# Kernel tuning notes

Measured on AMD Instinct MI355X. Metric: run time of the kernel, lower is better.

## Reference

```python
import jax, jax.numpy as jnp
import numpy as np

EPS = 1e-07
NUM_CLASSES = 46


def setup_inputs() -> dict:
    key = jax.random.key(0)
    k1, k2 = jax.random.split(key)
    N = 2_000_000
    y_pred = jax.random.uniform(k1, (N, NUM_CLASSES), dtype=jnp.float32)
    y_true = jax.random.randint(k2, (N,), 0, NUM_CLASSES, dtype=jnp.int64)
    return {"y_pred": y_pred, "y_true": y_true}


def reference(y_pred, y_true):
    # One fused pass replacing the 46-iteration Python loop.
    # onehot[n, c] = 1 if y_true[n] == c
    classes = jnp.arange(NUM_CLASSES, dtype=y_true.dtype)
    onehot = (y_true[:, None] == classes[None, :]).astype(y_pred.dtype)  # [N, C]

    col_sum = jnp.sum(y_pred, axis=0)                 # [C] = tp + fp per class
    tp = jnp.sum(onehot * y_pred, axis=0)             # [C]
    counts = jnp.sum(onehot, axis=0)                  # [C] = tp + fn per class

    fp = col_sum - tp
    fn = counts - tp

    precision = tp / (tp + fp + EPS)
    recall = tp / (tp + fn + EPS)
    f1 = 2.0 * precision * recall / (precision + recall + EPS)
    f1 = jnp.clip(f1, EPS, 1.0 - EPS)
    return 1.0 - jnp.mean(f1)
```

## Files before the change

kernel.cpp:

```cpp
#include <hip/hip_runtime.h>

#define EPSF 1e-7f
#define NCLS 46
#define BLOCK 256
#define GRID (23 * 72)

__global__ __launch_bounds__(BLOCK) void f1_partial(
    const float* __restrict__ yp,
    const int* __restrict__ yt,
    float* __restrict__ g_cs,
    float* __restrict__ g_tp,
    float* __restrict__ g_cnt,
    int n_rows)
{
    __shared__ float s_cs[NCLS], s_tp[NCLS], s_cnt[NCLS];
    const int tid = threadIdx.x;
    for (int i = tid; i < NCLS; i += BLOCK) { s_cs[i] = 0.f; s_tp[i] = 0.f; s_cnt[i] = 0.f; }
    __syncthreads();

    const int T  = BLOCK * GRID;
    const int t  = blockIdx.x * BLOCK + tid;
    const int s        = t % 23;
    const int rp0      = t / 23;
    const int rpstride = T / 23;
    const int npairs   = n_rows >> 1;

    int cls[4], hi[4];
    #pragma unroll
    for (int j = 0; j < 4; ++j) {
        int e  = 4 * s + j;
        hi[j]  = (e >= 46) ? 1 : 0;
        cls[j] = e - 46 * hi[j];
    }

    float cs[4] = {0.f,0.f,0.f,0.f};
    float tp[4] = {0.f,0.f,0.f,0.f};

    for (int rp = rp0; rp < npairs; rp += rpstride) {
        float4 v = *(const float4*)(yp + rp * 92 + 4 * s);
        int2 lab = *(const int2*)(yt + 2 * rp);
        float vv[4] = {v.x, v.y, v.z, v.w};
        #pragma unroll
        for (int j = 0; j < 4; ++j) {
            cs[j] += vv[j];
            int labj = hi[j] ? lab.y : lab.x;
            tp[j] += (labj == cls[j]) ? vv[j] : 0.f;
        }
    }

    #pragma unroll
    for (int j = 0; j < 4; ++j) {
        atomicAdd(&s_cs[cls[j]], cs[j]);
        atomicAdd(&s_tp[cls[j]], tp[j]);
    }

    for (int i = t; i < n_rows; i += T)
        atomicAdd(&s_cnt[yt[i]], 1.0f);

    if ((n_rows & 1) && blockIdx.x == 0 && tid < NCLS) {
        int L = n_rows - 1;
        float v = yp[L * NCLS + tid];
        atomicAdd(&s_cs[tid], v);
        if (yt[L] == tid) atomicAdd(&s_tp[tid], v);
    }

    __syncthreads();
    for (int i = tid; i < NCLS; i += BLOCK) {
        atomicAdd(&g_cs[i],  s_cs[i]);
        atomicAdd(&g_tp[i],  s_tp[i]);
        atomicAdd(&g_cnt[i], s_cnt[i]);
    }
}

__global__ void f1_final(const float* __restrict__ g_cs,
                         const float* __restrict__ g_tp,
                         const float* __restrict__ g_cnt,
                         float* __restrict__ out)
{
    const int lane = threadIdx.x;
    float f1 = 0.f;
    if (lane < NCLS) {
        float tp = g_tp[lane];
        float p  = tp / (g_cs[lane]  + EPSF);
        float r  = tp / (g_cnt[lane] + EPSF);
        float f  = 2.0f * p * r / (p + r + EPSF);
        f1 = fminf(fmaxf(f, EPSF), 1.0f - EPSF);
    }
    #pragma unroll
    for (int off = 32; off > 0; off >>= 1)
        f1 += __shfl_down(f1, off);
    if (lane == 0)
        out[0] = 1.0f - f1 * (1.0f / 46.0f);
}

extern "C" void kernel_launch(void* const* d_in, const int* in_sizes, int n_in,
                              void* d_out, int out_size, void* d_ws, size_t ws_size,
                              hipStream_t stream)
{
    const float* yp = (const float*)d_in[0];
    const int* yt   = (const int*)d_in[1];
    const int n_rows = in_sizes[1];

    float* g_cs  = (float*)d_ws;
    float* g_tp  = g_cs + NCLS;
    float* g_cnt = g_tp + NCLS;

    hipMemsetAsync(d_ws, 0, 3 * NCLS * sizeof(float), stream);
    f1_partial<<<GRID, BLOCK, 0, stream>>>(yp, yt, g_cs, g_tp, g_cnt, n_rows);
    f1_final<<<1, 64, 0, stream>>>(g_cs, g_tp, g_cnt, (float*)d_out);
}
```

Measured before the change: 524.0 us.

## Fuse finalize into reduction kernel via last-block ticket and inline label counting

Merges the final F1 computation into the partial-reduction kernel using a global atomic ticket, so the last block to finish computes the loss and the second kernel launch disappears. Label counts are now accumulated inside the main loop by the s==0 lane rather than in a separate pass over y_true. The grid grows and launch bounds request 8 blocks per CU. This adds extra threadfences and a global atomic per block, plus concentrated LDS atomic contention from the counting lanes.

```diff
diff --git a/kernel.cpp b/kernel.cpp
--- a/kernel.cpp
+++ b/kernel.cpp
@@ -3,23 +3,23 @@
 #define EPSF 1e-7f
 #define NCLS 46
 #define BLOCK 256
-#define GRID (23 * 72)
+#define GRID (23 * 88)
 
-__global__ __launch_bounds__(BLOCK) void f1_partial(
+__global__ __launch_bounds__(BLOCK, 8) void f1_fused(
     const float* __restrict__ yp,
     const int* __restrict__ yt,
-    float* __restrict__ g_cs,
-    float* __restrict__ g_tp,
-    float* __restrict__ g_cnt,
+    float* __restrict__ g,
+    float* __restrict__ out,
     int n_rows)
 {
     __shared__ float s_cs[NCLS], s_tp[NCLS], s_cnt[NCLS];
+    __shared__ int s_last;
     const int tid = threadIdx.x;
     for (int i = tid; i < NCLS; i += BLOCK) { s_cs[i] = 0.f; s_tp[i] = 0.f; s_cnt[i] = 0.f; }
     __syncthreads();
 
-    const int T  = BLOCK * GRID;
-    const int t  = blockIdx.x * BLOCK + tid;
+    const int T = BLOCK * GRID;
+    const int t = blockIdx.x * BLOCK + tid;
     const int s        = t % 23;
     const int rp0      = t / 23;
     const int rpstride = T / 23;
@@ -46,6 +46,10 @@
             int labj = hi[j] ? lab.y : lab.x;
             tp[j] += (labj == cls[j]) ? vv[j] : 0.f;
         }
+        if (s == 0) {
+            atomicAdd(&s_cnt[lab.x], 1.0f);
+            atomicAdd(&s_cnt[lab.y], 1.0f);
+        }
     }
 
     #pragma unroll
@@ -54,43 +58,44 @@
         atomicAdd(&s_tp[cls[j]], tp[j]);
     }
 
-    for (int i = t; i < n_rows; i += T)
-        atomicAdd(&s_cnt[yt[i]], 1.0f);
-
     if ((n_rows & 1) && blockIdx.x == 0 && tid < NCLS) {
         int L = n_rows - 1;
         float v = yp[L * NCLS + tid];
         atomicAdd(&s_cs[tid], v);
-        if (yt[L] == tid) atomicAdd(&s_tp[tid], v);
+        if (yt[L] == tid) { atomicAdd(&s_tp[tid], v); atomicAdd(&s_cnt[tid], 1.0f); }
     }
 
     __syncthreads();
     for (int i = tid; i < NCLS; i += BLOCK) {
-        atomicAdd(&g_cs[i],  s_cs[i]);
-        atomicAdd(&g_tp[i],  s_tp[i]);
-        atomicAdd(&g_cnt[i], s_cnt[i]);
+        atomicAdd(&g[i],          s_cs[i]);
+        atomicAdd(&g[NCLS + i],   s_tp[i]);
+        atomicAdd(&g[2*NCLS + i], s_cnt[i]);
     }
-}
 
-__global__ void f1_final(const float* __restrict__ g_cs,
-                         const float* __restrict__ g_tp,
-                         const float* __restrict__ g_cnt,
-                         float* __restrict__ out)
-{
-    const int lane = threadIdx.x;
-    float f1 = 0.f;
-    if (lane < NCLS) {
-        float tp = g_tp[lane];
-        float p  = tp / (g_cs[lane]  + EPSF);
-        float r  = tp / (g_cnt[lane] + EPSF);
-        float f  = 2.0f * p * r / (p + r + EPSF);
-        f1 = fminf(fmaxf(f, EPSF), 1.0f - EPSF);
+    __threadfence();
+    __syncthreads();
+    if (tid == 0) {
+        unsigned int ticket = atomicAdd((unsigned int*)&g[3*NCLS], 1u);
+        s_last = (ticket == (unsigned int)(gridDim.x - 1)) ? 1 : 0;
     }
-    #pragma unroll
-    for (int off = 32; off > 0; off >>= 1)
-        f1 += __shfl_down(f1, off);
-    if (lane == 0)
-        out[0] = 1.0f - f1 * (1.0f / 46.0f);
+    __syncthreads();
+    if (s_last && tid < 64) {
+        __threadfence();
+        volatile float* vg = g;
+        float f1 = 0.f;
+        if (tid < NCLS) {
+            float tpv = vg[NCLS + tid];
+            float p = tpv / (vg[tid]          + EPSF);
+            float r = tpv / (vg[2*NCLS + tid] + EPSF);
+            float f = 2.0f * p * r / (p + r + EPSF);
+            f1 = fminf(fmaxf(f, EPSF), 1.0f - EPSF);
+        }
+        #pragma unroll
+        for (int off = 32; off > 0; off >>= 1)
+            f1 += __shfl_down(f1, off);
+        if (tid == 0)
+            out[0] = 1.0f - f1 * (1.0f / 46.0f);
+    }
 }
 
 extern "C" void kernel_launch(void* const* d_in, const int* in_sizes, int n_in,
@@ -101,11 +106,6 @@
     const int* yt   = (const int*)d_in[1];
     const int n_rows = in_sizes[1];
 
-    float* g_cs  = (float*)d_ws;
-    float* g_tp  = g_cs + NCLS;
-    float* g_cnt = g_tp + NCLS;
-
-    hipMemsetAsync(d_ws, 0, 3 * NCLS * sizeof(float), stream);
-    f1_partial<<<GRID, BLOCK, 0, stream>>>(yp, yt, g_cs, g_tp, g_cnt, n_rows);
-    f1_final<<<1, 64, 0, stream>>>(g_cs, g_tp, g_cnt, (float*)d_out);
+    hipMemsetAsync(d_ws, 0, (3 * NCLS + 1) * sizeof(float), stream);
+    f1_fused<<<GRID, BLOCK, 0, stream>>>(yp, yt, (float*)d_ws, (float*)d_out, n_rows);
 }
```

Measured after the change: 630.6 us. 1.2x slower.
